# Optimization experiments

Hardware: AMD Instinct MI355X
Metric: run time of the kernel (lower is better)

The kernel has to match this reference:

```python
import jax, jax.numpy as jnp
import numpy as np

N_SRC, N_MID, N_DST = 200000, 40000, 8000
R = 4
E1, E2 = 1000000, 200000
IN_F, HID_F, OUT_F = 256, 128, 128


def setup_inputs() -> dict:
    key = jax.random.key(0)
    ks = jax.random.split(key, 10)
    x = jax.random.normal(ks[0], (N_SRC, IN_F), dtype=jnp.float32)
    W1 = jax.random.normal(ks[1], (R, IN_F, HID_F), dtype=jnp.float32) * 0.05
    b1 = jax.random.normal(ks[2], (R, HID_F), dtype=jnp.float32) * 0.05
    W2 = jax.random.normal(ks[3], (R, HID_F, OUT_F), dtype=jnp.float32) * 0.05
    b2 = jax.random.normal(ks[4], (R, OUT_F), dtype=jnp.float32) * 0.05
    src1 = jax.random.randint(ks[5], (R, E1), 0, N_SRC, dtype=jnp.int32)
    dst1 = jax.random.randint(ks[6], (R, E1), 0, N_MID, dtype=jnp.int32)
    src2 = jax.random.randint(ks[7], (R, E2), 0, N_MID, dtype=jnp.int32)
    dst2 = jax.random.randint(ks[8], (R, E2), 0, N_DST, dtype=jnp.int32)
    return {"x": x, "W1": W1, "b1": b1, "W2": W2, "b2": b2,
            "src1": src1, "dst1": dst1, "src2": src2, "dst2": dst2}


def _hetero_graphconv(h_src, W, b, src, dst, n_dst):
    """Sum over relations of GraphConv(norm='right'):
    per relation r: agg = scatter_add(dst, (h_src @ W[r])[src]); out_r = agg / in_deg + b[r]."""
    n_rel = W.shape[0]
    out = jnp.zeros((n_dst, W.shape[-1]), dtype=h_src.dtype)
    for r in range(n_rel):  # small fixed relation count
        m = h_src @ W[r]                                    # [N_src, F_out] (transform first: F_in >= F_out)
        msg = m[src[r]]                                     # [E, F_out] gather
        agg = jax.ops.segment_sum(msg, dst[r], num_segments=n_dst)
        deg = jax.ops.segment_sum(jnp.ones((src.shape[1],), dtype=h_src.dtype),
                                  dst[r], num_segments=n_dst)
        norm = jnp.where(deg > 0, 1.0 / deg, 0.0)           # norm='right', zero-degree -> 0
        out = out + agg * norm[:, None] + b[r]
    return out


def reference(x, W1, b1, W2, b2, src1, dst1, src2, dst2):
    h = _hetero_graphconv(x, W1, b1, src1, dst1, N_MID)     # layer 1 -> [N_MID, HID_F]
    out = _hetero_graphconv(h, W2, b2, src2, dst2, N_DST)   # layer 2 -> [N_DST, OUT_F]
    return out
```

## Files before the change

kernel.cpp:

```cpp
#include <hip/hip_runtime.h>
#include <hip/hip_bf16.h>

#define N_SRC  200000
#define N_MIDN 40000
#define N_DSTN 8000
#define RREL   4
#define E1N    1000000
#define E2N    200000
#define CAP    96
#define EPB    8192
#define NB1C   123
#define NB2C   25
#define NPAD2  8064

typedef __attribute__((ext_vector_type(8))) short bf16x8;
typedef __attribute__((ext_vector_type(4))) float f32x4;
typedef __attribute__((ext_vector_type(2))) float f32x2;
typedef __attribute__((ext_vector_type(4))) unsigned short u16x4;

__device__ __forceinline__ unsigned short f2bf(float f) {
    unsigned int u = __float_as_uint(f);
    u = (u + 0x7FFFu + ((u >> 16) & 1u)) >> 16;
    return (unsigned short)u;
}

__device__ __forceinline__ float bflo(unsigned int u) { return __uint_as_float(u << 16); }
__device__ __forceinline__ float bfhi(unsigned int u) { return __uint_as_float(u & 0xFFFF0000u); }

__device__ __forceinline__ void gload_lds16(const void* g, void* l) {
    __builtin_amdgcn_global_load_lds((const __attribute__((address_space(1))) void*)g,
                                     (__attribute__((address_space(3))) void*)l, 16, 0, 0);
}

template<int K>
__device__ __forceinline__ void convwf_body(
    int id, const float* __restrict__ W, unsigned short* __restrict__ WtF)
{
    constexpr int KS = K / 32;
    if (id >= RREL * KS * 8 * 64) return;
    int lane = id & 63;
    int fi   = id >> 6;
    int nblk = fi & 7;
    int rk   = fi >> 3;
    int kki  = rk & (KS - 1);
    int rr   = rk / KS;
    int n  = nblk * 16 + (lane & 15);
    int k0 = kki * 32 + (lane >> 4) * 8;
    unsigned short* op = WtF + (size_t)id * 8;
    #pragma unroll
    for (int j = 0; j < 8; ++j)
        op[j] = f2bf(W[((size_t)(rr * K + k0 + j)) * 128 + n]);
}

__global__ __launch_bounds__(256) void fusedpre_kernel(
    const int* __restrict__ dst1, unsigned char* __restrict__ rank81,
    unsigned int* __restrict__ hist1,
    const int* __restrict__ dst2, unsigned char* __restrict__ rank82,
    unsigned int* __restrict__ hist2,
    const float* __restrict__ W1, unsigned short* __restrict__ wt1,
    const float* __restrict__ W2, unsigned short* __restrict__ wt2)
{
    __shared__ unsigned int cnt4[10240];
    const int bid = blockIdx.x;
    const int tid = threadIdx.x;
    const int NCNT = 4 * NB1C + 4 * NB2C;

    if (bid < NCNT) {
        const int* dst; unsigned char* rank8; unsigned int* hist;
        int epr, ndst4, nb, r, b, sb = bid;
        if (sb < 4 * NB1C) {
            r = sb / NB1C; b = sb - r * NB1C;
            dst = dst1; rank8 = rank81; hist = hist1;
            epr = E1N; ndst4 = N_MIDN / 4; nb = NB1C;
        } else {
            sb -= 4 * NB1C;
            r = sb / NB2C; b = sb - r * NB2C;
            dst = dst2; rank8 = rank82; hist = hist2;
            epr = E2N; ndst4 = N_DSTN / 4; nb = NB2C;
        }
        for (int i = tid; i < ndst4; i += 256) cnt4[i] = 0;
        __syncthreads();
        const int e0 = b * EPB;
        const int ne = min(EPB, epr - e0);
        const int* dp = dst + (size_t)r * epr + e0;
        unsigned char* rp = rank8 + (size_t)r * epr + e0;
        for (int i = tid; i < ne; i += 256) {
            int d = dp[i];
            unsigned int sh = (d & 3) * 8;
            unsigned int old = atomicAdd(&cnt4[d >> 2], 1u << sh);
            rp[i] = (unsigned char)((old >> sh) & 0xFFu);
        }
        __syncthreads();
        unsigned int* hp = hist + ((size_t)r * nb + b) * ndst4;
        for (int i = tid; i < ndst4; i += 256) hp[i] = cnt4[i];
        return;
    }
    int b2 = bid - NCNT;
    if (b2 < 64) { convwf_body<256>(b2 * 256 + tid, W1, wt1); return; }
    convwf_body<128>((b2 - 64) * 256 + tid, W2, wt2);
}

__global__ __launch_bounds__(256) void fusedscan_kernel(
    unsigned int* __restrict__ hist1, int* __restrict__ cnt1,
    unsigned int* __restrict__ hist2, int* __restrict__ cnt2)
{
    const int NS1 = (RREL * N_MIDN + 255) / 256;
    unsigned int* hist; int* cnt; int ndst, ndst4, nb, id;
    if (blockIdx.x < NS1) {
        hist = hist1; cnt = cnt1; ndst = N_MIDN; ndst4 = N_MIDN / 4; nb = NB1C;
        id = blockIdx.x * 256 + threadIdx.x;
    } else {
        hist = hist2; cnt = cnt2; ndst = N_DSTN; ndst4 = N_DSTN / 4; nb = NB2C;
        id = (blockIdx.x - NS1) * 256 + threadIdx.x;
    }
    if (id >= RREL * ndst) return;
    int r = id / ndst;
    int node = id - r * ndst;
    unsigned char* hb = (unsigned char*)hist;
    const size_t stride = (size_t)ndst4 * 4;
    unsigned char* p0 = hb + (size_t)r * nb * stride + node;
    unsigned int run = 0;
    for (int b = 0; b < nb; ++b) {
        unsigned char* pp = p0 + (size_t)b * stride;
        unsigned int c = *pp;
        *pp = (unsigned char)run;
        run += c;
    }
    cnt[id] = (int)run;
}

__global__ __launch_bounds__(512, 4) void fusedmain_kernel(
    const float* __restrict__ X,
    const unsigned short* __restrict__ WtF,
    unsigned char* __restrict__ Mout, int M, int nscat,
    const int* __restrict__ src1, const int* __restrict__ dst1,
    const unsigned char* __restrict__ rank81, const unsigned int* __restrict__ hist1,
    int* __restrict__ ell1,
    const int* __restrict__ src2, const int* __restrict__ dst2,
    const unsigned char* __restrict__ rank82, const unsigned int* __restrict__ hist2,
    int* __restrict__ ell2)
{
    __shared__ char lds[40960];
    const int bid = blockIdx.x;
    const int tid = threadIdx.x;

    if (bid < nscat) {
        int sb = bid;
        const int* src; const int* dst; const unsigned char* rank8;
        const unsigned int* hist; int* ell; int epr, ndst4, nb, r, b;
        if (sb < 4 * NB1C) {
            r = sb / NB1C; b = sb - r * NB1C;
            src = src1; dst = dst1; rank8 = rank81; hist = hist1; ell = ell1;
            epr = E1N; ndst4 = N_MIDN / 4; nb = NB1C;
        } else {
            sb -= 4 * NB1C;
            r = sb / NB2C; b = sb - r * NB2C;
            src = src2; dst = dst2; rank8 = rank82; hist = hist2; ell = ell2;
            epr = E2N; ndst4 = N_DSTN / 4; nb = NB2C;
        }
        unsigned int* pre4 = (unsigned int*)lds;
        const unsigned int* hp = hist + ((size_t)r * nb + b) * ndst4;
        for (int i = tid; i < ndst4; i += 512) pre4[i] = hp[i];
        __syncthreads();
        const int e0 = b * EPB;
        const int ne = min(EPB, epr - e0);
        const size_t eb = (size_t)r * epr + e0;
        const unsigned char* pre = (const unsigned char*)pre4;
        const int ndst = ndst4 * 4;
        for (int i = tid; i < ne; i += 512) {
            int d = dst[eb + i];
            int s = src[eb + i];
            int slot = (int)rank8[eb + i] + (int)pre[d];
            if (slot < CAP) ell[((size_t)r * ndst + d) * CAP + slot] = s;
        }
        return;
    }

    unsigned short* As = (unsigned short*)lds;
    const int m0 = (bid - nscat) * 64;

    float4 v[8];
    #pragma unroll
    for (int j = 0; j < 8; ++j) {
        int slot = j * 512 + tid;
        int row = slot >> 6, col4 = slot & 63;
        int grow = m0 + row; if (grow >= M) grow = M - 1;
        v[j] = *(const float4*)&X[(size_t)grow * 256 + col4 * 4];
    }
    #pragma unroll
    for (int j = 0; j < 8; ++j) {
        int slot = j * 512 + tid;
        int row = slot >> 6, col4 = slot & 63;
        int h   = col4 >> 5, c4l = col4 & 31;
        u16x4 o;
        o.x = f2bf(v[j].x); o.y = f2bf(v[j].y);
        o.z = f2bf(v[j].z); o.w = f2bf(v[j].w);
        int bb  = c4l * 8;
        int off = (((bb >> 4) ^ (row & 7)) << 4) | (bb & 15);
        *(u16x4*)((char*)As + h * 16384 + row * 256 + off) = o;
    }
    __syncthreads();

    const int lane = tid & 63;
    const int wave = tid >> 6;
    const int r    = wave & 3;
    const int nh   = (wave >> 2) & 1;
    const int wn   = nh * 64;
    const int lr   = lane & 15;
    const int kg   = lane >> 4;
    const int xorv = (lr & 7) << 4;
    const unsigned short* Wr = WtF + (size_t)r * 8 * 8 * 512;

    f32x4 acc[4][4] = {};
    #pragma unroll
    for (int h = 0; h < 2; ++h) {
        const char* Ap = (const char*)As + h * 16384;
        #pragma unroll
        for (int ks = 0; ks < 4; ++ks) {
            bf16x8 af[4], bv[4];
            const int kb = (ks * 64 + kg * 16) ^ xorv;
            #pragma unroll
            for (int mi = 0; mi < 4; ++mi)
                af[mi] = *(const bf16x8*)(Ap + (mi * 16 + lr) * 256 + kb);
            const int kk32 = h * 4 + ks;
            #pragma unroll
            for (int ni = 0; ni < 4; ++ni)
                bv[ni] = *(const bf16x8*)&Wr[((size_t)kk32 * 8 + nh * 4 + ni) * 512 + lane * 8];
            #pragma unroll
            for (int mi = 0; mi < 4; ++mi)
                #pragma unroll
                for (int ni = 0; ni < 4; ++ni)
                    acc[mi][ni] = __builtin_amdgcn_mfma_f32_16x16x32_bf16(
                        af[mi], bv[ni], acc[mi][ni], 0, 0, 0);
        }
    }

    const int rowoff = (lane >> 4) * 4;
    #pragma unroll
    for (int mi = 0; mi < 4; ++mi) {
        #pragma unroll
        for (int j = 0; j < 4; ++j) {
            int grow = m0 + mi * 16 + rowoff + j;
            if (grow < M) {
                #pragma unroll
                for (int ni = 0; ni < 4; ++ni) {
                    int pk = __builtin_amdgcn_cvt_pk_fp8_f32(
                        acc[mi][ni][j], acc[mi][ni][j], 0, false);
                    Mout[(size_t)grow * 512 + r * 128 + wn + ni * 16 + lr]
                        = (unsigned char)(pk & 0xFF);
                }
            }
        }
    }
}

__global__ __launch_bounds__(256) void gather1_kernel(
    const unsigned char* __restrict__ Mt,
    const int* __restrict__ ell, const int* __restrict__ cnt,
    const float* __restrict__ bias,
    unsigned short* __restrict__ outp, int ndst)
{
    __shared__ float red[RREL][2][128];
    const int node = blockIdx.x;
    const int lane = threadIdx.x & 63;
    const int r    = threadIdx.x >> 6;
    const int half = lane >> 5;
    const int sub  = lane & 31;
    const int idx  = r * ndst + node;
    const int c    = cnt[idx];
    const int deg  = c < CAP ? c : CAP;
    const int base = idx * CAP;
    const int coff = r * 128 + sub * 4;

    float a0 = 0.f, a1 = 0.f, a2 = 0.f, a3 = 0.f;
    int e = 0;
#define ACC8(vv)                                            \
    {                                                       \
        f32x2 lo = __builtin_amdgcn_cvt_pk_f32_fp8(vv, false); \
        f32x2 hi = __builtin_amdgcn_cvt_pk_f32_fp8(vv, true);  \
        a0 += lo.x; a1 += lo.y; a2 += hi.x; a3 += hi.y;     \
    }
    for (; e + 16 <= deg; e += 16) {
        int4 sa = *(const int4*)&ell[base + e];
        int4 sb = *(const int4*)&ell[base + e + 4];
        int4 sc = *(const int4*)&ell[base + e + 8];
        int4 sd = *(const int4*)&ell[base + e + 12];
        int s0 = half ? sa.y : sa.x;
        int s1 = half ? sa.w : sa.z;
        int s2 = half ? sb.y : sb.x;
        int s3 = half ? sb.w : sb.z;
        int s4 = half ? sc.y : sc.x;
        int s5 = half ? sc.w : sc.z;
        int s6 = half ? sd.y : sd.x;
        int s7 = half ? sd.w : sd.z;
        unsigned int v0 = *(const unsigned int*)&Mt[(size_t)s0 * 512 + coff];
        unsigned int v1 = *(const unsigned int*)&Mt[(size_t)s1 * 512 + coff];
        unsigned int v2 = *(const unsigned int*)&Mt[(size_t)s2 * 512 + coff];
        unsigned int v3 = *(const unsigned int*)&Mt[(size_t)s3 * 512 + coff];
        unsigned int v4 = *(const unsigned int*)&Mt[(size_t)s4 * 512 + coff];
        unsigned int v5 = *(const unsigned int*)&Mt[(size_t)s5 * 512 + coff];
        unsigned int v6 = *(const unsigned int*)&Mt[(size_t)s6 * 512 + coff];
        unsigned int v7 = *(const unsigned int*)&Mt[(size_t)s7 * 512 + coff];
        ACC8(v0) ACC8(v1) ACC8(v2) ACC8(v3)
        ACC8(v4) ACC8(v5) ACC8(v6) ACC8(v7)
    }
    for (; e + 8 <= deg; e += 8) {
        int4 sa = *(const int4*)&ell[base + e];
        int4 sb = *(const int4*)&ell[base + e + 4];
        int s0 = half ? sa.y : sa.x;
        int s1 = half ? sa.w : sa.z;
        int s2 = half ? sb.y : sb.x;
        int s3 = half ? sb.w : sb.z;
        unsigned int v0 = *(const unsigned int*)&Mt[(size_t)s0 * 512 + coff];
        unsigned int v1 = *(const unsigned int*)&Mt[(size_t)s1 * 512 + coff];
        unsigned int v2 = *(const unsigned int*)&Mt[(size_t)s2 * 512 + coff];
        unsigned int v3 = *(const unsigned int*)&Mt[(size_t)s3 * 512 + coff];
        ACC8(v0) ACC8(v1) ACC8(v2) ACC8(v3)
    }
    for (; e < deg; e += 2) {
        int s0 = ell[base + e];
        int s1 = (e + 1 < deg) ? ell[base + e + 1] : -1;
        int s = half ? s1 : s0;
        if (s >= 0) {
            unsigned int vv = *(const unsigned int*)&Mt[(size_t)s * 512 + coff];
            ACC8(vv)
        }
    }
#undef ACC8
    float norm = c > 0 ? 1.0f / (float)c : 0.0f;
    red[r][half][sub * 4 + 0] = a0 * norm;
    red[r][half][sub * 4 + 1] = a1 * norm;
    red[r][half][sub * 4 + 2] = a2 * norm;
    red[r][half][sub * 4 + 3] = a3 * norm;
    __syncthreads();

    const int tt = threadIdx.x;
    if (tt < 128) {
        float s = red[0][0][tt] + red[0][1][tt] + red[1][0][tt] + red[1][1][tt]
                + red[2][0][tt] + red[2][1][tt] + red[3][0][tt] + red[3][1][tt]
                + bias[tt] + bias[128 + tt] + bias[256 + tt] + bias[384 + tt];
        outp[(size_t)node * 128 + tt] = f2bf(s);
    }
}

__global__ __launch_bounds__(256) void gather2h_kernel(
    const unsigned short* __restrict__ H,
    const int* __restrict__ ell, const int* __restrict__ cnt,
    unsigned short* __restrict__ agg2, int ndst)
{
    __shared__ float red[RREL][2][128];
    const int node = blockIdx.x;
    const int lane = threadIdx.x & 63;
    const int r    = threadIdx.x >> 6;
    const int half = lane >> 5;
    const int sub  = lane & 31;
    const int idx  = r * ndst + node;
    const int c    = cnt[idx];
    const int deg  = c < CAP ? c : CAP;
    const int base = idx * CAP;
    const int coff = sub * 4;

    float a0 = 0.f, a1 = 0.f, a2 = 0.f, a3 = 0.f;
    int e = 0;
    for (; e + 8 <= deg; e += 8) {
        int4 sa = *(const int4*)&ell[base + e];
        int4 sb = *(const int4*)&ell[base + e + 4];
        int sA = half ? sa.y : sa.x;
        int sB = half ? sa.w : sa.z;
        int sC = half ? sb.y : sb.x;
        int sD = half ? sb.w : sb.z;
        uint2 v0 = *(const uint2*)&H[(size_t)sA * 128 + coff];
        uint2 v1 = *(const uint2*)&H[(size_t)sB * 128 + coff];
        uint2 v2 = *(const uint2*)&H[(size_t)sC * 128 + coff];
        uint2 v3 = *(const uint2*)&H[(size_t)sD * 128 + coff];
        a0 += bflo(v0.x) + bflo(v1.x) + bflo(v2.x) + bflo(v3.x);
        a1 += bfhi(v0.x) + bfhi(v1.x) + bfhi(v2.x) + bfhi(v3.x);
        a2 += bflo(v0.y) + bflo(v1.y) + bflo(v2.y) + bflo(v3.y);
        a3 += bfhi(v0.y) + bfhi(v1.y) + bfhi(v2.y) + bfhi(v3.y);
    }
    for (; e < deg; e += 2) {
        int s0 = ell[base + e];
        int s1 = (e + 1 < deg) ? ell[base + e + 1] : -1;
        int s = half ? s1 : s0;
        if (s >= 0) {
            uint2 v = *(const uint2*)&H[(size_t)s * 128 + coff];
            a0 += bflo(v.x); a1 += bfhi(v.x);
            a2 += bflo(v.y); a3 += bfhi(v.y);
        }
    }
    float norm = c > 0 ? 1.0f / (float)c : 0.0f;
    red[r][half][sub * 4 + 0] = a0 * norm;
    red[r][half][sub * 4 + 1] = a1 * norm;
    red[r][half][sub * 4 + 2] = a2 * norm;
    red[r][half][sub * 4 + 3] = a3 * norm;
    __syncthreads();

    const int t  = threadIdx.x;
    const int tt = t & 127;
    const int swz = ((((tt >> 3) ^ (node & 7)) << 3) | (tt & 7));
    #pragma unroll
    for (int q = 0; q < 2; ++q) {
        int rr = (t >> 7) + q * 2;
        float val = red[rr][0][tt] + red[rr][1][tt];
        agg2[((size_t)rr * NPAD2 + node) * 128 + swz] = f2bf(val);
    }
}

__global__ __launch_bounds__(256, 1) void gemm2p_kernel(
    const unsigned short* __restrict__ agg2,
    const unsigned short* __restrict__ WtF,
    const float* __restrict__ b2,
    float* __restrict__ outp, int M)
{
    __shared__ unsigned short As[4 * 128 * 128];

    const int m0  = blockIdx.x * 128;
    const int tid = threadIdx.x;

    #pragma unroll
    for (int rr = 0; rr < 4; ++rr) {
        #pragma unroll
        for (int j = 0; j < 8; ++j) {
            int L = j * 4096 + tid * 16;
            int row  = L >> 8;
            int boff = L & 255;
            gload_lds16((const char*)agg2 + ((size_t)rr * NPAD2 + m0 + row) * 256 + boff,
                        (char*)As + rr * 32768 + L);
        }
    }
    __syncthreads();

    const int lane = tid & 63;
    const int wave = tid >> 6;
    const int mh   = wave & 1;
    const int nh   = wave >> 1;
    const int wm   = mh * 64;
    const int wn   = nh * 64;
    const int lr   = lane & 15;
    const int kg   = lane >> 4;
    const int xorv = (lr & 7) << 4;

    f32x4 acc[4][4] = {};
    #pragma unroll
    for (int rr = 0; rr < 4; ++rr) {
        const char* Ap = (const char*)As + rr * 32768;
        const unsigned short* Wr = WtF + (size_t)rr * 4 * 8 * 512;
        #pragma unroll
        for (int ks = 0; ks < 4; ++ks) {
            bf16x8 af[4], bv[4];
            const int kb = (ks * 64 + kg * 16) ^ xorv;
            #pragma unroll
            for (int mi = 0; mi < 4; ++mi)
                af[mi] = *(const bf16x8*)(Ap + (wm + mi * 16 + lr) * 256 + kb);
            #pragma unroll
            for (int ni = 0; ni < 4; ++ni)
                bv[ni] = *(const bf16x8*)&Wr[((size_t)ks * 8 + nh * 4 + ni) * 512 + lane * 8];
            #pragma unroll
            for (int mi = 0; mi < 4; ++mi)
                #pragma unroll
                for (int ni = 0; ni < 4; ++ni)
                    acc[mi][ni] = __builtin_amdgcn_mfma_f32_16x16x32_bf16(
                        af[mi], bv[ni], acc[mi][ni], 0, 0, 0);
        }
    }

    const int rowoff = (lane >> 4) * 4;
    float bsum[4];
    #pragma unroll
    for (int ni = 0; ni < 4; ++ni) {
        int col = wn + ni * 16 + lr;
        bsum[ni] = b2[col] + b2[128 + col] + b2[256 + col] + b2[384 + col];
    }
    #pragma unroll
    for (int mi = 0; mi < 4; ++mi) {
        #pragma unroll
        for (int j = 0; j < 4; ++j) {
            int grow = m0 + wm + mi * 16 + rowoff + j;
            if (grow < M) {
                #pragma unroll
                for (int ni = 0; ni < 4; ++ni)
                    outp[(size_t)grow * 128 + wn + ni * 16 + lr]
                        = acc[mi][ni][j] + bsum[ni];
            }
        }
    }
}

extern "C" void kernel_launch(void* const* d_in, const int* in_sizes, int n_in,
                              void* d_out, int out_size, void* d_ws, size_t ws_size,
                              hipStream_t stream)
{
    const float* x  = (const float*)d_in[0];
    const float* W1 = (const float*)d_in[1];
    const float* b1 = (const float*)d_in[2];
    const float* W2 = (const float*)d_in[3];
    const float* b2 = (const float*)d_in[4];
    const int* src1 = (const int*)d_in[5];
    const int* dst1 = (const int*)d_in[6];
    const int* src2 = (const int*)d_in[7];
    const int* dst2 = (const int*)d_in[8];

    char* p = (char*)d_ws;
    auto alloc = [&](size_t bytes) {
        char* q = p; p += (bytes + 255) & ~(size_t)255; return q;
    };
    unsigned char*  m1    = (unsigned char*)alloc((size_t)N_SRC * 512);
    int*            ell1  = (int*)alloc((size_t)RREL * N_MIDN * CAP * 4);
    int*            cnt1  = (int*)alloc((size_t)RREL * N_MIDN * 4);
    unsigned short* h     = (unsigned short*)alloc((size_t)N_MIDN * 128 * 2);
    unsigned short* wt1   = (unsigned short*)alloc((size_t)RREL * 8 * 8 * 64 * 8 * 2);
    unsigned short* wt2   = (unsigned short*)alloc((size_t)RREL * 4 * 8 * 64 * 8 * 2);
    unsigned int*   hist1 = (unsigned int*)alloc((size_t)NB1C * RREL * (N_MIDN / 4) * 4);
    unsigned char*  rank81= (unsigned char*)alloc((size_t)RREL * E1N);
    unsigned int*   hist2 = (unsigned int*)alloc((size_t)NB2C * RREL * (N_DSTN / 4) * 4);
    unsigned char*  rank82= (unsigned char*)alloc((size_t)RREL * E2N);
    int*            ell2  = (int*)alloc((size_t)RREL * N_DSTN * CAP * 4);
    int*            cnt2  = (int*)alloc((size_t)RREL * N_DSTN * 4);
    unsigned short* agg2  = (unsigned short*)m1;

    const int NCNT = 4 * NB1C + 4 * NB2C;
    fusedpre_kernel<<<NCNT + 96, 256, 0, stream>>>(
        dst1, rank81, hist1, dst2, rank82, hist2, W1, wt1, W2, wt2);

    const int NS1 = (RREL * N_MIDN + 255) / 256;
    const int NS2 = (RREL * N_DSTN + 255) / 256;
    fusedscan_kernel<<<NS1 + NS2, 256, 0, stream>>>(hist1, cnt1, hist2, cnt2);

    const int NSCAT = NCNT;
    const int NGEMM = (N_SRC + 63) / 64;
    fusedmain_kernel<<<NSCAT + NGEMM, 512, 0, stream>>>(
        x, wt1, m1, N_SRC, NSCAT,
        src1, dst1, rank81, hist1, ell1,
        src2, dst2, rank82, hist2, ell2);

    gather1_kernel<<<N_MIDN, 256, 0, stream>>>(m1, ell1, cnt1, b1, h, N_MIDN);

    gather2h_kernel<<<N_DSTN, 256, 0, stream>>>(h, ell2, cnt2, agg2, N_DSTN);
    gemm2p_kernel<<<(N_DSTN + 127) / 128, 256, 0, stream>>>(agg2, wt2, b2, (float*)d_out, N_DSTN);
}
```

Before: 392.1 us.

## Replace fixed-capacity ELL adjacency with compact CSR offsets via prefix scan

```diff
diff --git a/kernel.cpp b/kernel.cpp
--- a/kernel.cpp
+++ b/kernel.cpp
@@ -7,10 +7,11 @@
 #define RREL   4
 #define E1N    1000000
 #define E2N    200000
-#define CAP    96
 #define EPB    8192
 #define NB1C   123
 #define NB2C   25
+#define NSB1   625
+#define NSB2   125
 #define NPAD2  8064
 
 typedef __attribute__((ext_vector_type(8))) short bf16x8;
@@ -102,18 +103,21 @@
 
 __global__ __launch_bounds__(256) void fusedscan_kernel(
     unsigned int* __restrict__ hist1, int* __restrict__ cnt1,
-    unsigned int* __restrict__ hist2, int* __restrict__ cnt2)
-{
-    const int NS1 = (RREL * N_MIDN + 255) / 256;
-    unsigned int* hist; int* cnt; int ndst, ndst4, nb, id;
-    if (blockIdx.x < NS1) {
-        hist = hist1; cnt = cnt1; ndst = N_MIDN; ndst4 = N_MIDN / 4; nb = NB1C;
-        id = blockIdx.x * 256 + threadIdx.x;
+    int* __restrict__ toff1, int* __restrict__ btot1,
+    unsigned int* __restrict__ hist2, int* __restrict__ cnt2,
+    int* __restrict__ toff2, int* __restrict__ btot2)
+{
+    __shared__ int sc[256];
+    const int tid = threadIdx.x;
+    unsigned int* hist; int* cnt; int* toff; int* btot; int ndst, ndst4, nb, lb;
+    if (blockIdx.x < NSB1) {
+        hist = hist1; cnt = cnt1; toff = toff1; btot = btot1;
+        ndst = N_MIDN; ndst4 = N_MIDN / 4; nb = NB1C; lb = blockIdx.x;
     } else {
-        hist = hist2; cnt = cnt2; ndst = N_DSTN; ndst4 = N_DSTN / 4; nb = NB2C;
-        id = (blockIdx.x - NS1) * 256 + threadIdx.x;
-    }
-    if (id >= RREL * ndst) return;
+        hist = hist2; cnt = cnt2; toff = toff2; btot = btot2;
+        ndst = N_DSTN; ndst4 = N_DSTN / 4; nb = NB2C; lb = blockIdx.x - NSB1;
+    }
+    const int id = lb * 256 + tid;
     int r = id / ndst;
     int node = id - r * ndst;
     unsigned char* hb = (unsigned char*)hist;
@@ -127,6 +131,63 @@
         run += c;
     }
     cnt[id] = (int)run;
+    int pad = (int)((run + 3u) & ~3u);
+
+    int v = pad;
+    sc[tid] = v;
+    __syncthreads();
+    #pragma unroll
+    for (int off = 1; off < 256; off <<= 1) {
+        int t = (tid >= off) ? sc[tid - off] : 0;
+        __syncthreads();
+        v += t;
+        sc[tid] = v;
+        __syncthreads();
+    }
+    toff[id] = v - pad;
+    if (tid == 255) btot[lb] = v;
+}
+
+__global__ __launch_bounds__(1024) void bscan_kernel(
+    int* __restrict__ btot1, int* __restrict__ btot2)
+{
+    __shared__ int s[1024];
+    const int tid = threadIdx.x;
+    int v = (tid < NSB1) ? btot1[tid] : 0;
+    int o = v;
+    s[tid] = v; __syncthreads();
+    #pragma unroll
+    for (int off = 1; off < 1024; off <<= 1) {
+        int t = (tid >= off) ? s[tid - off] : 0;
+        __syncthreads();
+        v += t; s[tid] = v; __syncthreads();
+    }
+    if (tid < NSB1) btot1[tid] = v - o;
+    __syncthreads();
+    int v2 = (tid < NSB2) ? btot2[tid] : 0;
+    int o2 = v2;
+    s[tid] = v2; __syncthreads();
+    #pragma unroll
+    for (int off = 1; off < 1024; off <<= 1) {
+        int t = (tid >= off) ? s[tid - off] : 0;
+        __syncthreads();
+        v2 += t; s[tid] = v2; __syncthreads();
+    }
+    if (tid < NSB2) btot2[tid] = v2 - o2;
+}
+
+__global__ __launch_bounds__(256) void finoff_kernel(
+    const int* __restrict__ toff1, const int* __restrict__ btot1, int* __restrict__ offs1,
+    const int* __restrict__ toff2, const int* __restrict__ btot2, int* __restrict__ offs2)
+{
+    if (blockIdx.x < NSB1) {
+        int id = blockIdx.x * 256 + threadIdx.x;
+        offs1[id] = btot1[blockIdx.x] + toff1[id];
+    } else {
+        int lb = blockIdx.x - NSB1;
+        int id = lb * 256 + threadIdx.x;
+        offs2[id] = btot2[lb] + toff2[id];
+    }
 }
 
 __global__ __launch_bounds__(512, 4) void fusedmain_kernel(
@@ -135,10 +196,10 @@
     unsigned char* __restrict__ Mout, int M, int nscat,
     const int* __restrict__ src1, const int* __restrict__ dst1,
     const unsigned char* __restrict__ rank81, const unsigned int* __restrict__ hist1,
-    int* __restrict__ ell1,
+    const int* __restrict__ offs1, int* __restrict__ ell1,
     const int* __restrict__ src2, const int* __restrict__ dst2,
     const unsigned char* __restrict__ rank82, const unsigned int* __restrict__ hist2,
-    int* __restrict__ ell2)
+    const int* __restrict__ offs2, int* __restrict__ ell2)
 {
     __shared__ char lds[40960];
     const int bid = blockIdx.x;
@@ -147,15 +208,18 @@
     if (bid < nscat) {
         int sb = bid;
         const int* src; const int* dst; const unsigned char* rank8;
-        const unsigned int* hist; int* ell; int epr, ndst4, nb, r, b;
+        const unsigned int* hist; const int* offs; int* ell;
+        int epr, ndst4, nb, r, b;
         if (sb < 4 * NB1C) {
             r = sb / NB1C; b = sb - r * NB1C;
-            src = src1; dst = dst1; rank8 = rank81; hist = hist1; ell = ell1;
+            src = src1; dst = dst1; rank8 = rank81; hist = hist1;
+            offs = offs1; ell = ell1;
             epr = E1N; ndst4 = N_MIDN / 4; nb = NB1C;
         } else {
             sb -= 4 * NB1C;
             r = sb / NB2C; b = sb - r * NB2C;
-            src = src2; dst = dst2; rank8 = rank82; hist = hist2; ell = ell2;
+            src = src2; dst = dst2; rank8 = rank82; hist = hist2;
+            offs = offs2; ell = ell2;
             epr = E2N; ndst4 = N_DSTN / 4; nb = NB2C;
         }
         unsigned int* pre4 = (unsigned int*)lds;
@@ -171,7 +235,7 @@
             int d = dst[eb + i];
             int s = src[eb + i];
             int slot = (int)rank8[eb + i] + (int)pre[d];
-            if (slot < CAP) ell[((size_t)r * ndst + d) * CAP + slot] = s;
+            ell[offs[r * ndst + d] + slot] = s;
         }
         return;
     }
@@ -256,7 +320,8 @@
 
 __global__ __launch_bounds__(256) void gather1_kernel(
     const unsigned char* __restrict__ Mt,
-    const int* __restrict__ ell, const int* __restrict__ cnt,
+    const int* __restrict__ ell, const int* __restrict__ offs,
+    const int* __restrict__ cnt,
     const float* __restrict__ bias,
     unsigned short* __restrict__ outp, int ndst)
 {
@@ -268,8 +333,8 @@
     const int sub  = lane & 31;
     const int idx  = r * ndst + node;
     const int c    = cnt[idx];
-    const int deg  = c < CAP ? c : CAP;
-    const int base = idx * CAP;
+    const int deg  = c;
+    const int base = offs[idx];
     const int coff = r * 128 + sub * 4;
 
     float a0 = 0.f, a1 = 0.f, a2 = 0.f, a3 = 0.f;
@@ -345,7 +410,8 @@
 
 __global__ __launch_bounds__(256) void gather2h_kernel(
     const unsigned short* __restrict__ H,
-    const int* __restrict__ ell, const int* __restrict__ cnt,
+    const int* __restrict__ ell, const int* __restrict__ offs,
+    const int* __restrict__ cnt,
     unsigned short* __restrict__ agg2, int ndst)
 {
     __shared__ float red[RREL][2][128];
@@ -356,8 +422,8 @@
     const int sub  = lane & 31;
     const int idx  = r * ndst + node;
     const int c    = cnt[idx];
-    const int deg  = c < CAP ? c : CAP;
-    const int base = idx * CAP;
+    const int deg  = c;
+    const int base = offs[idx];
     const int coff = sub * 4;
 
     float a0 = 0.f, a1 = 0.f, a2 = 0.f, a3 = 0.f;
@@ -505,8 +571,11 @@
         char* q = p; p += (bytes + 255) & ~(size_t)255; return q;
     };
     unsigned char*  m1    = (unsigned char*)alloc((size_t)N_SRC * 512);
-    int*            ell1  = (int*)alloc((size_t)RREL * N_MIDN * CAP * 4);
+    int*            ell1  = (int*)alloc(((size_t)RREL * E1N + 4 * RREL * N_MIDN) * 4);
     int*            cnt1  = (int*)alloc((size_t)RREL * N_MIDN * 4);
+    int*            toff1 = (int*)alloc((size_t)RREL * N_MIDN * 4);
+    int*            offs1 = (int*)alloc((size_t)RREL * N_MIDN * 4);
+    int*            btot1 = (int*)alloc(1024 * 4);
     unsigned short* h     = (unsigned short*)alloc((size_t)N_MIDN * 128 * 2);
     unsigned short* wt1   = (unsigned short*)alloc((size_t)RREL * 8 * 8 * 64 * 8 * 2);
     unsigned short* wt2   = (unsigned short*)alloc((size_t)RREL * 4 * 8 * 64 * 8 * 2);
@@ -514,27 +583,32 @@
     unsigned char*  rank81= (unsigned char*)alloc((size_t)RREL * E1N);
     unsigned int*   hist2 = (unsigned int*)alloc((size_t)NB2C * RREL * (N_DSTN / 4) * 4);
     unsigned char*  rank82= (unsigned char*)alloc((size_t)RREL * E2N);
-    int*            ell2  = (int*)alloc((size_t)RREL * N_DSTN * CAP * 4);
+    int*            ell2  = (int*)alloc(((size_t)RREL * E2N + 4 * RREL * N_DSTN) * 4);
     int*            cnt2  = (int*)alloc((size_t)RREL * N_DSTN * 4);
+    int*            toff2 = (int*)alloc((size_t)RREL * N_DSTN * 4);
+    int*            offs2 = (int*)alloc((size_t)RREL * N_DSTN * 4);
+    int*            btot2 = (int*)alloc(1024 * 4);
     unsigned short* agg2  = (unsigned short*)m1;
 
     const int NCNT = 4 * NB1C + 4 * NB2C;
     fusedpre_kernel<<<NCNT + 96, 256, 0, stream>>>(
         dst1, rank81, hist1, dst2, rank82, hist2, W1, wt1, W2, wt2);
 
-    const int NS1 = (RREL * N_MIDN + 255) / 256;
-    const int NS2 = (RREL * N_DSTN + 255) / 256;
-    fusedscan_kernel<<<NS1 + NS2, 256, 0, stream>>>(hist1, cnt1, hist2, cnt2);
+    fusedscan_kernel<<<NSB1 + NSB2, 256, 0, stream>>>(
+        hist1, cnt1, toff1, btot1, hist2, cnt2, toff2, btot2);
+    bscan_kernel<<<1, 1024, 0, stream>>>(btot1, btot2);
+    finoff_kernel<<<NSB1 + NSB2, 256, 0, stream>>>(
+        toff1, btot1, offs1, toff2, btot2, offs2);
 
     const int NSCAT = NCNT;
     const int NGEMM = (N_SRC + 63) / 64;
     fusedmain_kernel<<<NSCAT + NGEMM, 512, 0, stream>>>(
         x, wt1, m1, N_SRC, NSCAT,
-        src1, dst1, rank81, hist1, ell1,
-        src2, dst2, rank82, hist2, ell2);
-
-    gather1_kernel<<<N_MIDN, 256, 0, stream>>>(m1, ell1, cnt1, b1, h, N_MIDN);
-
-    gather2h_kernel<<<N_DSTN, 256, 0, stream>>>(h, ell2, cnt2, agg2, N_DSTN);
+        src1, dst1, rank81, hist1, offs1, ell1,
+        src2, dst2, rank82, hist2, offs2, ell2);
+
+    gather1_kernel<<<N_MIDN, 256, 0, stream>>>(m1, ell1, offs1, cnt1, b1, h, N_MIDN);
+
+    gather2h_kernel<<<N_DSTN, 256, 0, stream>>>(h, ell2, offs2, cnt2, agg2, N_DSTN);
     gemm2p_kernel<<<(N_DSTN + 127) / 128, 256, 0, stream>>>(agg2, wt2, b2, (float*)d_out, N_DSTN);
 }
```

Result: slower. 414.9 us (+5.8%).
